# Kernel tuning notes

Hardware: AMD Instinct MI355X
Metric: run time of the kernel (lower is better)

The kernel has to match this reference:

```python
import jax, jax.numpy as jnp
import numpy as np
import math

D_MODEL = 1024
NUM_HEADS = 16
HEAD_DIM = D_MODEL // NUM_HEADS


def setup_inputs() -> dict:
    key = jax.random.key(0)
    ks = jax.random.split(key, 9)
    B, S = 2, 2048
    scale = 1.0 / math.sqrt(D_MODEL)
    x = jax.random.normal(ks[0], (B, S, D_MODEL), dtype=jnp.float32)
    # torch nn.Linear params: weight [out, in], bias [out]
    Wq = jax.random.normal(ks[1], (D_MODEL, D_MODEL), dtype=jnp.float32) * scale
    bq = jax.random.normal(ks[2], (D_MODEL,), dtype=jnp.float32) * scale
    Wk = jax.random.normal(ks[3], (D_MODEL, D_MODEL), dtype=jnp.float32) * scale
    bk = jax.random.normal(ks[4], (D_MODEL,), dtype=jnp.float32) * scale
    Wv = jax.random.normal(ks[5], (D_MODEL, D_MODEL), dtype=jnp.float32) * scale
    bv = jax.random.normal(ks[6], (D_MODEL,), dtype=jnp.float32) * scale
    Wo = jax.random.normal(ks[7], (D_MODEL, D_MODEL), dtype=jnp.float32) * scale
    bo = jax.random.normal(ks[8], (D_MODEL,), dtype=jnp.float32) * scale
    return {"x": x, "Wq": Wq, "bq": bq, "Wk": Wk, "bk": bk,
            "Wv": Wv, "bv": bv, "Wo": Wo, "bo": bo}


def reference(x, Wq, bq, Wk, bk, Wv, bv, Wo, bo):
    B, S, _ = x.shape
    H, Dh = NUM_HEADS, HEAD_DIM

    def proj(W, b):
        # torch Linear: x @ W.T + b -> [B,S,D] -> [B,H,S,Dh]
        y = jnp.einsum('bsd,ed->bse', x, W) + b
        return y.reshape(B, S, H, Dh).transpose(0, 2, 1, 3)

    Q = proj(Wq, bq)
    K = proj(Wk, bk)
    V = proj(Wv, bv)

    # scores [B,H,S,S], causal mask with -inf, then scale by 1/sqrt(head_dim)
    scores = jnp.einsum('bhqd,bhkd->bhqk', Q, K)
    causal = jnp.tril(jnp.ones((S, S), dtype=bool))
    scores = jnp.where(causal, scores, -jnp.inf)
    A = jax.nn.softmax(scores / math.sqrt(Dh), axis=-1)

    O = jnp.einsum('bhqk,bhkd->bhqd', A, V)  # [B,H,S,Dh]
    O = O.transpose(0, 2, 1, 3).reshape(B, S, H * Dh)
    return jnp.einsum('bsd,ed->bse', O, Wo) + bo
```

## Files before the change

### kernel.cpp

```cpp
#include <hip/hip_runtime.h>


typedef _Float16 f16x8 __attribute__((ext_vector_type(8)));
typedef _Float16 f16x4 __attribute__((ext_vector_type(4)));
typedef float f32x4 __attribute__((ext_vector_type(4)));

#define S_  2048
#define DM  1024
#define NH  16
#define DH  64

__device__ __forceinline__ void gload_lds16(const void* g, void* s) {
  __builtin_amdgcn_global_load_lds(
      (const __attribute__((address_space(1))) void*)g,
      (__attribute__((address_space(3))) void*)s, 16, 0, 0);
}


__global__ void cvt_x_kernel(const float* __restrict__ src,
                             _Float16* __restrict__ dst) {
  const int i = blockIdx.x * 256 + threadIdx.x;
  const float4 v = ((const float4*)src)[i];
  f16x4 h;
  h[0] = (_Float16)v.x; h[1] = (_Float16)v.y;
  h[2] = (_Float16)v.z; h[3] = (_Float16)v.w;
  ((f16x4*)dst)[i] = h;
}

__global__ void cvt_w_kernel(const float* __restrict__ w0,
                             const float* __restrict__ w1,
                             const float* __restrict__ w2,
                             const float* __restrict__ w3,
                             _Float16* __restrict__ dst) {
  const int y = blockIdx.y;
  const float* src = (y == 0) ? w0 : (y == 1) ? w1 : (y == 2) ? w2 : w3;
  const int i = blockIdx.x * 256 + threadIdx.x;
  const float4 v = ((const float4*)src)[i];
  f16x4 h;
  h[0] = (_Float16)v.x; h[1] = (_Float16)v.y;
  h[2] = (_Float16)v.z; h[3] = (_Float16)v.w;
  ((f16x4*)(dst + (size_t)y * (DM * DM)))[i] = h;
}


__device__ __forceinline__ void gemm_core_k1024(
    const _Float16* __restrict__ A, const _Float16* __restrict__ W,
    _Float16* As, _Float16* Ws, f32x4 acc[4][4], int m0, int n0)
{
  const int t = threadIdx.x;
  const int w = t >> 6, l = t & 63;
  const int quad = l >> 4, ln = l & 15;
  const int wm = (w >> 1) << 6, wn = (w & 1) << 6;
  const int srow = l >> 2, scol = (l & 3) << 3;

  for (int k0 = 0; k0 < DM; k0 += 32) {
#pragma unroll
    for (int i = 0; i < 2; ++i) {
      const int ra = w * 32 + i * 16;
      gload_lds16(&A[(size_t)(m0 + ra + srow) * DM + k0 + scol], &As[ra * 32]);
      gload_lds16(&W[(size_t)(n0 + ra + srow) * DM + k0 + scol], &Ws[ra * 32]);
    }
    __syncthreads();

    f16x8 af[4], bf[4];
#pragma unroll
    for (int mi = 0; mi < 4; ++mi)
      af[mi] = *(const f16x8*)&As[(wm + mi * 16 + ln) * 32 + quad * 8];
#pragma unroll
    for (int ni = 0; ni < 4; ++ni)
      bf[ni] = *(const f16x8*)&Ws[(wn + ni * 16 + ln) * 32 + quad * 8];
#pragma unroll
    for (int mi = 0; mi < 4; ++mi)
#pragma unroll
      for (int ni = 0; ni < 4; ++ni)
        acc[mi][ni] = __builtin_amdgcn_mfma_f32_16x16x32_f16(
            af[mi], bf[ni], acc[mi][ni], 0, 0, 0);
    __syncthreads();
  }
}

__global__ __launch_bounds__(256, 2) void gemm_qkv_kernel(
    const _Float16* __restrict__ xb, const _Float16* __restrict__ wb,
    const float* __restrict__ bq, const float* __restrict__ bk,
    const float* __restrict__ bv, _Float16* __restrict__ qkv)
{
  __shared__ _Float16 As[128 * 32];
  __shared__ _Float16 Ws[128 * 32];
  const int z = blockIdx.z;
  const _Float16* W = wb + (size_t)z * (DM * DM);
  const float* bias = (z == 0) ? bq : ((z == 1) ? bk : bv);
  _Float16* out = qkv + (size_t)z * 4194304;

  const f32x4 z4 = {0.f, 0.f, 0.f, 0.f};
  f32x4 acc[4][4];
#pragma unroll
  for (int mi = 0; mi < 4; ++mi)
#pragma unroll
    for (int ni = 0; ni < 4; ++ni) acc[mi][ni] = z4;

  const int m0 = blockIdx.y * 128, n0 = blockIdx.x * 128;
  gemm_core_k1024(xb, W, As, Ws, acc, m0, n0);

  const int t = threadIdx.x, w = t >> 6, l = t & 63;
  const int quad = l >> 4, ln = l & 15;
  const int wm = (w >> 1) << 6, wn = (w & 1) << 6;
  const float scale = (z == 0) ? 0.18033688f : 1.0f;

#pragma unroll
  for (int ni = 0; ni < 4; ++ni) {
    const int c = n0 + wn + ni * 16 + ln;
    const float bias_c = bias[c];
    const int h = c >> 6, d = c & 63;
#pragma unroll
    for (int mi = 0; mi < 4; ++mi) {
      const int mb = m0 + wm + mi * 16 + quad * 4;
#pragma unroll
      for (int r = 0; r < 4; ++r) {
        const int mg = mb + r;
        const int b = mg >> 11, s = mg & 2047;
        const int bh = b * NH + h;
        const float v = (acc[mi][ni][r] + bias_c) * scale;
        size_t idx;
        if (z == 2)
          idx = (size_t)bh * 131072 + (s >> 5) * 2048 + (d >> 4) * 512 +
                ((s >> 3) & 3) * 128 + (d & 15) * 8 + (s & 7);
        else
          idx = (size_t)bh * 131072 + (s >> 4) * 1024 + (d >> 5) * 512 +
                ((d >> 3) & 3) * 128 + (s & 15) * 8 + (d & 7);
        out[idx] = (_Float16)v;
      }
    }
  }
}

__global__ __launch_bounds__(256, 2) void gemm_out_kernel(
    const _Float16* __restrict__ ob, const _Float16* __restrict__ wo,
    const float* __restrict__ bo, float* __restrict__ out)
{
  __shared__ _Float16 As[128 * 32];
  __shared__ _Float16 Ws[128 * 32];
  const f32x4 z4 = {0.f, 0.f, 0.f, 0.f};
  f32x4 acc[4][4];
#pragma unroll
  for (int mi = 0; mi < 4; ++mi)
#pragma unroll
    for (int ni = 0; ni < 4; ++ni) acc[mi][ni] = z4;

  const int m0 = blockIdx.y * 128, n0 = blockIdx.x * 128;
  gemm_core_k1024(ob, wo, As, Ws, acc, m0, n0);

  const int t = threadIdx.x, w = t >> 6, l = t & 63;
  const int quad = l >> 4, ln = l & 15;
  const int wm = (w >> 1) << 6, wn = (w & 1) << 6;

#pragma unroll
  for (int ni = 0; ni < 4; ++ni) {
    const int c = n0 + wn + ni * 16 + ln;
    const float bias_c = bo[c];
#pragma unroll
    for (int mi = 0; mi < 4; ++mi) {
      const int mb = m0 + wm + mi * 16 + quad * 4;
#pragma unroll
      for (int r = 0; r < 4; ++r)
        out[(size_t)(mb + r) * DM + c] = acc[mi][ni][r] + bias_c;
    }
  }
}


struct KVfrag { f16x8 k[4]; f16x8 v[4]; };

__device__ __forceinline__ KVfrag load_tile(const _Float16* __restrict__ kb_,
                                            const _Float16* __restrict__ vb_,
                                            int t, int l) {
  KVfrag f;
#pragma unroll
  for (int i = 0; i < 4; ++i)
    f.k[i] = *(const f16x8*)(kb_ + (size_t)(t * 4 + i) * 512 + l * 8);
#pragma unroll
  for (int i = 0; i < 4; ++i)
    f.v[i] = *(const f16x8*)(vb_ + (size_t)(t * 4 + i) * 512 + l * 8);
  return f;
}

template <bool DIAG>
__device__ __forceinline__ void compute_tile(
    const KVfrag& kv, const f16x8 (&qf)[2][2], f32x4 (&oacc)[4][2],
    float (&l_i)[2], _Float16* Ps, int quad, int ln)
{
  const f32x4 z4 = {0.f, 0.f, 0.f, 0.f};
  f32x4 sacc[2][2];
#pragma unroll
  for (int mi = 0; mi < 2; ++mi)
#pragma unroll
    for (int qc = 0; qc < 2; ++qc) sacc[mi][qc] = z4;

#pragma unroll
  for (int ks = 0; ks < 2; ++ks)
#pragma unroll
    for (int mi = 0; mi < 2; ++mi)
#pragma unroll
      for (int qc = 0; qc < 2; ++qc)
        sacc[mi][qc] = __builtin_amdgcn_mfma_f32_16x16x32_f16(
            kv.k[mi * 2 + ks], qf[qc][ks], sacc[mi][qc], 0, 0, 0);

#pragma unroll
  for (int qc = 0; qc < 2; ++qc) {
    float rs = 0.f;
#pragma unroll
    for (int mi = 0; mi < 2; ++mi) {
      float p[4];
#pragma unroll
      for (int r = 0; r < 4; ++r) {
        p[r] = exp2f(sacc[mi][qc][r]);
        if (DIAG && (mi * 16 + quad * 4 + r > qc * 16 + ln)) p[r] = 0.f;
        rs += p[r];
      }
      f16x4 pk;
      pk[0] = (_Float16)p[0]; pk[1] = (_Float16)p[1];
      pk[2] = (_Float16)p[2]; pk[3] = (_Float16)p[3];
      *(f16x4*)&Ps[(qc * 16 + ln) * 40 + mi * 16 + quad * 4] = pk;
    }
    rs += __shfl_xor(rs, 16);
    rs += __shfl_xor(rs, 32);
    l_i[qc] += rs;
  }

  f16x8 pb[2];
#pragma unroll
  for (int qc = 0; qc < 2; ++qc)
    pb[qc] = *(const f16x8*)&Ps[(qc * 16 + ln) * 40 + quad * 8];

#pragma unroll
  for (int di = 0; di < 4; ++di)
#pragma unroll
    for (int qc = 0; qc < 2; ++qc)
      oacc[di][qc] = __builtin_amdgcn_mfma_f32_16x16x32_f16(
          kv.v[di], pb[qc], oacc[di][qc], 0, 0, 0);
}

__global__ __launch_bounds__(64) void attn_kernel(
    const _Float16* __restrict__ QF, const _Float16* __restrict__ KF,
    const _Float16* __restrict__ VF, _Float16* __restrict__ Ob)
{
  __shared__ _Float16 Ps[2 * 16 * 40];

  const int i = blockIdx.x;
  const int jj = i >> 3;
  const int bh = (i & 7) + ((jj & 3) << 3);
  const int qw = 63 - (jj >> 2);
  const int q0 = qw << 5;

  const int l = threadIdx.x, quad = l >> 4, ln = l & 15;
  const _Float16* kb_ = KF + (size_t)bh * 131072;
  const _Float16* vb_ = VF + (size_t)bh * 131072;
  const _Float16* qb_ = QF + (size_t)bh * 131072;

  f16x8 qf[2][2];
#pragma unroll
  for (int qc = 0; qc < 2; ++qc)
#pragma unroll
    for (int ks = 0; ks < 2; ++ks)
      qf[qc][ks] = *(const f16x8*)
          (qb_ + (size_t)((2 * qw + qc) * 2 + ks) * 512 + l * 8);

  const f32x4 z4 = {0.f, 0.f, 0.f, 0.f};
  f32x4 oacc[4][2];
#pragma unroll
  for (int di = 0; di < 4; ++di)
#pragma unroll
    for (int qc = 0; qc < 2; ++qc) oacc[di][qc] = z4;
  float l_i[2] = {0.f, 0.f};

  const int ntf = q0 >> 5;
  KVfrag b0 = load_tile(kb_, vb_, 0, l);
  KVfrag b1;
  for (int t = 0; t < ntf; ++t) {
    if ((t & 1) == 0) {
      b1 = load_tile(kb_, vb_, t + 1, l);
      compute_tile<false>(b0, qf, oacc, l_i, Ps, quad, ln);
    } else {
      b0 = load_tile(kb_, vb_, t + 1, l);
      compute_tile<false>(b1, qf, oacc, l_i, Ps, quad, ln);
    }
  }
  if (ntf & 1) compute_tile<true>(b1, qf, oacc, l_i, Ps, quad, ln);
  else         compute_tile<true>(b0, qf, oacc, l_i, Ps, quad, ln);

  const int bidx = bh >> 4, h = bh & 15;
#pragma unroll
  for (int qc = 0; qc < 2; ++qc) {
    const float inv = 1.0f / l_i[qc];
    const int q = q0 + qc * 16 + ln;
    _Float16* orow = Ob + (size_t)(bidx * S_ + q) * DM + h * DH + quad * 4;
#pragma unroll
    for (int di = 0; di < 4; ++di) {
      f16x4 o4;
#pragma unroll
      for (int r = 0; r < 4; ++r) o4[r] = (_Float16)(oacc[di][qc][r] * inv);
      *(f16x4*)(orow + di * 16) = o4;
    }
  }
}


extern "C" void kernel_launch(void* const* d_in, const int* in_sizes, int n_in,
                              void* d_out, int out_size, void* d_ws, size_t ws_size,
                              hipStream_t stream) {
  (void)in_sizes; (void)n_in; (void)out_size; (void)ws_size;
  const float* x  = (const float*)d_in[0];
  const float* Wq = (const float*)d_in[1];
  const float* bq = (const float*)d_in[2];
  const float* Wk = (const float*)d_in[3];
  const float* bk = (const float*)d_in[4];
  const float* Wv = (const float*)d_in[5];
  const float* bv = (const float*)d_in[6];
  const float* Wo = (const float*)d_in[7];
  const float* bo = (const float*)d_in[8];

  char* ws = (char*)d_ws;
  _Float16* xb  = (_Float16*)(ws);
  _Float16* wb  = (_Float16*)(ws + (8u << 20));
  _Float16* qkv = (_Float16*)(ws + (16u << 20));
  _Float16* ob  = (_Float16*)(ws + (40u << 20));

  cvt_x_kernel<<<dim3(4096), dim3(256), 0, stream>>>(x, xb);
  cvt_w_kernel<<<dim3(1024, 4), dim3(256), 0, stream>>>(Wq, Wk, Wv, Wo, wb);
  gemm_qkv_kernel<<<dim3(8, 32, 3), dim3(256), 0, stream>>>(xb, wb, bq, bk, bv, qkv);
  attn_kernel<<<dim3(2048), dim3(64), 0, stream>>>(
      qkv, qkv + 4194304, qkv + 2 * 4194304, ob);
  gemm_out_kernel<<<dim3(8, 32), dim3(256), 0, stream>>>(
      ob, wb + (size_t)3 * DM * DM, bo, (float*)d_out);
}
```

Before: 207.2 us.

## Split KV tiles across two waves with pairing of causal query blocks

The attention kernel now runs two waves per block. Each wave handles alternating KV tiles for the same query block, and the partial outputs and row sums are merged through shared memory. Each block processes a long and a short causal query block (63-p and p) to balance work. Also swizzles the P staging layout to reduce LDS bank conflicts, and uses the raw hardware exp2 and packed round-toward-zero f16 conversion. This is meant to shorten the per-block critical path and balance the causal load, at the cost of extra syncs and a shared-memory merge.

```diff
diff --git a/kernel.cpp b/kernel.cpp
--- a/kernel.cpp
+++ b/kernel.cpp
@@ -3,6 +3,7 @@
 
 typedef _Float16 f16x8 __attribute__((ext_vector_type(8)));
 typedef _Float16 f16x4 __attribute__((ext_vector_type(4)));
+typedef _Float16 f16x2 __attribute__((ext_vector_type(2)));
 typedef float f32x4 __attribute__((ext_vector_type(4)));
 
 #define S_  2048
@@ -14,6 +15,10 @@
   __builtin_amdgcn_global_load_lds(
       (const __attribute__((address_space(1))) void*)g,
       (__attribute__((address_space(3))) void*)s, 16, 0, 0);
+}
+
+__device__ __forceinline__ f16x2 pkrtz(float a, float b) {
+  return __builtin_bit_cast(f16x2, __builtin_amdgcn_cvt_pkrtz(a, b));
 }
 
 
@@ -204,6 +209,7 @@
         sacc[mi][qc] = __builtin_amdgcn_mfma_f32_16x16x32_f16(
             kv.k[mi * 2 + ks], qf[qc][ks], sacc[mi][qc], 0, 0, 0);
 
+  const int sw = (ln & 3) << 1;
 #pragma unroll
   for (int qc = 0; qc < 2; ++qc) {
     float rs = 0.f;
@@ -212,14 +218,15 @@
       float p[4];
 #pragma unroll
       for (int r = 0; r < 4; ++r) {
-        p[r] = exp2f(sacc[mi][qc][r]);
+        p[r] = __builtin_amdgcn_exp2f(sacc[mi][qc][r]);
         if (DIAG && (mi * 16 + quad * 4 + r > qc * 16 + ln)) p[r] = 0.f;
         rs += p[r];
       }
-      f16x4 pk;
-      pk[0] = (_Float16)p[0]; pk[1] = (_Float16)p[1];
-      pk[2] = (_Float16)p[2]; pk[3] = (_Float16)p[3];
-      *(f16x4*)&Ps[(qc * 16 + ln) * 40 + mi * 16 + quad * 4] = pk;
+      const f16x2 lo = pkrtz(p[0], p[1]);
+      const f16x2 hi = pkrtz(p[2], p[3]);
+      const f16x4 pk = __builtin_shufflevector(lo, hi, 0, 1, 2, 3);
+      const int g = (mi * 4 + quad) ^ sw;
+      *(f16x4*)&Ps[(qc * 16 + ln) * 40 + g * 4] = pk;
     }
     rs += __shfl_xor(rs, 16);
     rs += __shfl_xor(rs, 32);
@@ -228,8 +235,10 @@
 
   f16x8 pb[2];
 #pragma unroll
-  for (int qc = 0; qc < 2; ++qc)
-    pb[qc] = *(const f16x8*)&Ps[(qc * 16 + ln) * 40 + quad * 8];
+  for (int qc = 0; qc < 2; ++qc) {
+    const int g2 = (quad * 2) ^ sw;
+    pb[qc] = *(const f16x8*)&Ps[(qc * 16 + ln) * 40 + g2 * 4];
+  }
 
 #pragma unroll
   for (int di = 0; di < 4; ++di)
@@ -239,67 +248,100 @@
           kv.v[di], pb[qc], oacc[di][qc], 0, 0, 0);
 }
 
-__global__ __launch_bounds__(64) void attn_kernel(
+__global__ __launch_bounds__(128, 2) void attn_kernel(
     const _Float16* __restrict__ QF, const _Float16* __restrict__ KF,
     const _Float16* __restrict__ VF, _Float16* __restrict__ Ob)
 {
-  __shared__ _Float16 Ps[2 * 16 * 40];
+  __shared__ _Float16 Ps[2 * 32 * 40];
+  __shared__ float mrg[64 * 34];
 
   const int i = blockIdx.x;
-  const int jj = i >> 3;
-  const int bh = (i & 7) + ((jj & 3) << 3);
-  const int qw = 63 - (jj >> 2);
-  const int q0 = qw << 5;
-
-  const int l = threadIdx.x, quad = l >> 4, ln = l & 15;
+  const int bh = ((i & 7) << 2) | ((i >> 3) & 3);
+  const int p = i >> 5;
+
+  const int tid = threadIdx.x;
+  const int w = tid >> 6, l = tid & 63;
+  const int quad = l >> 4, ln = l & 15;
+
+  const _Float16* qb_ = QF + (size_t)bh * 131072;
   const _Float16* kb_ = KF + (size_t)bh * 131072;
   const _Float16* vb_ = VF + (size_t)bh * 131072;
-  const _Float16* qb_ = QF + (size_t)bh * 131072;
-
-  f16x8 qf[2][2];
-#pragma unroll
-  for (int qc = 0; qc < 2; ++qc)
-#pragma unroll
-    for (int ks = 0; ks < 2; ++ks)
-      qf[qc][ks] = *(const f16x8*)
-          (qb_ + (size_t)((2 * qw + qc) * 2 + ks) * 512 + l * 8);
+  _Float16* psw = Ps + w * (32 * 40);
+  const int bidx = bh >> 4, h = bh & 15;
 
   const f32x4 z4 = {0.f, 0.f, 0.f, 0.f};
-  f32x4 oacc[4][2];
-#pragma unroll
-  for (int di = 0; di < 4; ++di)
-#pragma unroll
-    for (int qc = 0; qc < 2; ++qc) oacc[di][qc] = z4;
-  float l_i[2] = {0.f, 0.f};
-
-  const int ntf = q0 >> 5;
-  KVfrag b0 = load_tile(kb_, vb_, 0, l);
-  KVfrag b1;
-  for (int t = 0; t < ntf; ++t) {
-    if ((t & 1) == 0) {
-      b1 = load_tile(kb_, vb_, t + 1, l);
-      compute_tile<false>(b0, qf, oacc, l_i, Ps, quad, ln);
-    } else {
-      b0 = load_tile(kb_, vb_, t + 1, l);
-      compute_tile<false>(b1, qf, oacc, l_i, Ps, quad, ln);
-    }
-  }
-  if (ntf & 1) compute_tile<true>(b1, qf, oacc, l_i, Ps, quad, ln);
-  else         compute_tile<true>(b0, qf, oacc, l_i, Ps, quad, ln);
-
-  const int bidx = bh >> 4, h = bh & 15;
-#pragma unroll
-  for (int qc = 0; qc < 2; ++qc) {
-    const float inv = 1.0f / l_i[qc];
-    const int q = q0 + qc * 16 + ln;
-    _Float16* orow = Ob + (size_t)(bidx * S_ + q) * DM + h * DH + quad * 4;
-#pragma unroll
-    for (int di = 0; di < 4; ++di) {
-      f16x4 o4;
-#pragma unroll
-      for (int r = 0; r < 4; ++r) o4[r] = (_Float16)(oacc[di][qc][r] * inv);
-      *(f16x4*)(orow + di * 16) = o4;
-    }
+
+#pragma unroll
+  for (int mem = 0; mem < 2; ++mem) {
+    const int qw = (mem == 0) ? (63 - p) : p;
+    const int q0 = qw << 5;
+
+    f16x8 qf[2][2];
+#pragma unroll
+    for (int qc = 0; qc < 2; ++qc)
+#pragma unroll
+      for (int ks = 0; ks < 2; ++ks)
+        qf[qc][ks] = *(const f16x8*)
+            (qb_ + (size_t)((2 * qw + qc) * 2 + ks) * 512 + l * 8);
+
+    f32x4 oacc[4][2];
+#pragma unroll
+    for (int di = 0; di < 4; ++di)
+#pragma unroll
+      for (int qc = 0; qc < 2; ++qc) oacc[di][qc] = z4;
+    float l_i[2] = {0.f, 0.f};
+
+    const int n = (qw >= w) ? (((qw - w) >> 1) + 1) : 0;
+    if (n > 0) {
+      KVfrag b0 = load_tile(kb_, vb_, w, l);
+      KVfrag b1;
+      for (int k = 0; k + 1 < n; ++k) {
+        const int tnext = w + 2 * (k + 1);
+        if ((k & 1) == 0) {
+          b1 = load_tile(kb_, vb_, tnext, l);
+          compute_tile<false>(b0, qf, oacc, l_i, psw, quad, ln);
+        } else {
+          b0 = load_tile(kb_, vb_, tnext, l);
+          compute_tile<false>(b1, qf, oacc, l_i, psw, quad, ln);
+        }
+      }
+      const KVfrag& last = ((n - 1) & 1) ? b1 : b0;
+      if (((qw - w) & 1) == 0)
+        compute_tile<true>(last, qf, oacc, l_i, psw, quad, ln);
+      else
+        compute_tile<false>(last, qf, oacc, l_i, psw, quad, ln);
+    }
+
+    if (w == 1) {
+#pragma unroll
+      for (int di = 0; di < 4; ++di)
+#pragma unroll
+        for (int qc = 0; qc < 2; ++qc)
+#pragma unroll
+          for (int r = 0; r < 4; ++r)
+            mrg[l * 34 + di * 8 + qc * 4 + r] = oacc[di][qc][r];
+#pragma unroll
+      for (int qc = 0; qc < 2; ++qc) mrg[l * 34 + 32 + qc] = l_i[qc];
+    }
+    __syncthreads();
+    if (w == 0) {
+#pragma unroll
+      for (int qc = 0; qc < 2; ++qc) {
+        const float inv = 1.0f / (l_i[qc] + mrg[l * 34 + 32 + qc]);
+        const int q = q0 + qc * 16 + ln;
+        _Float16* orow = Ob + (size_t)(bidx * S_ + q) * DM + h * DH + quad * 4;
+#pragma unroll
+        for (int di = 0; di < 4; ++di) {
+          f16x4 o4;
+#pragma unroll
+          for (int r = 0; r < 4; ++r)
+            o4[r] = (_Float16)((oacc[di][qc][r] +
+                                mrg[l * 34 + di * 8 + qc * 4 + r]) * inv);
+          *(f16x4*)(orow + di * 16) = o4;
+        }
+      }
+    }
+    __syncthreads();
   }
 }
 
@@ -327,7 +369,7 @@
   cvt_x_kernel<<<dim3(4096), dim3(256), 0, stream>>>(x, xb);
   cvt_w_kernel<<<dim3(1024, 4), dim3(256), 0, stream>>>(Wq, Wk, Wv, Wo, wb);
   gemm_qkv_kernel<<<dim3(8, 32, 3), dim3(256), 0, stream>>>(xb, wb, bq, bk, bv, qkv);
-  attn_kernel<<<dim3(2048), dim3(64), 0, stream>>>(
+  attn_kernel<<<dim3(1024), dim3(128), 0, stream>>>(
       qkv, qkv + 4194304, qkv + 2 * 4194304, ob);
   gemm_out_kernel<<<dim3(8, 32), dim3(256), 0, stream>>>(
       ob, wb + (size_t)3 * DM * DM, bo, (float*)d_out);
```

Result: faster. 185.0 us (-10.7%).
